# Performance work log

Hardware: AMD Instinct MI355X
Metric: run time of the kernel (lower is better)

Reference implementation:

```python
import jax, jax.numpy as jnp
import numpy as np

EPS = 1e-9
# exp factors for iterations i = 4,3,2,1,0,-1,-2 ; i == -2 -> 0.0
EXP_FACTORS = np.array([-(4.0 ** i) if i != -2 else 0.0 for i in range(4, -3, -1)], dtype=np.float32)


def setup_inputs() -> dict:
    key = jax.random.key(0)
    k1, k2 = jax.random.split(key)
    B, N, D = 16, 2048, 256
    preds = jax.random.normal(k1, (B, N, D), dtype=jnp.float32)
    labels = jax.random.normal(k2, (B, N, D), dtype=jnp.float32)
    return {"preds": preds, "labels": labels}


def _pairwise_dist(p1, p2):
    # [B,N,1] + [B,1,N] - 2 * p1 @ p2^T -> [B,N,N]
    p1_norm = jnp.sum(p1 * p1, axis=-1)[..., :, None]
    p2_norm = jnp.sum(p2 * p2, axis=-1)[..., None, :]
    return p1_norm + p2_norm - 2.0 * jnp.einsum('bnd,bmd->bnm', p1, p2)


def _approx_match(pwdist):
    B, N, _ = pwdist.shape
    match0 = jnp.zeros_like(pwdist)
    currency0 = jnp.ones((B, N, 1), dtype=pwdist.dtype)
    cost0 = jnp.ones((B, 1, N), dtype=pwdist.dtype)

    def body(carry, exp_factor):
        match, cost, currency = carry
        bids = jnp.exp(exp_factor * pwdist) * cost              # [B,N,N]
        bids = bids * currency / (jnp.sum(bids, axis=2, keepdims=True) + EPS)
        bid_wt = jnp.minimum(cost / (jnp.sum(bids, axis=1, keepdims=True) + EPS), 1.0)
        bids = bids * bid_wt
        match = match + bids
        cost = jnp.maximum(cost - jnp.sum(bids, axis=1, keepdims=True), 0.0)
        currency = jnp.maximum(currency - jnp.sum(bids, axis=2, keepdims=True), 0.0)
        return (match, cost, currency), None

    (match, _, _), _ = jax.lax.scan(body, (match0, cost0, currency0), jnp.asarray(EXP_FACTORS))
    return match


def reference(preds, labels):
    pwdist = _pairwise_dist(preds, labels)
    match = _approx_match(pwdist)
    return jnp.sum(match * pwdist)
```

## Files before the change

### kernel.cpp

```cpp
#include <hip/hip_runtime.h>
#include <cstdint>

#define B_ 16
#define N_ 2048
#define D_ 256
#define EPS_ 1e-9f

#define AS1 __attribute__((address_space(1)))
#define AS3 __attribute__((address_space(3)))

typedef float f4 __attribute__((ext_vector_type(4)));
typedef __attribute__((ext_vector_type(8))) short short8;

__device__ inline unsigned short f2bf(float x){
  unsigned int u = __float_as_uint(x);
  u = (u + 0x7fffu + ((u >> 16) & 1u)) >> 16;
  return (unsigned short)u;
}
__device__ inline float bf2f(unsigned short u){
  return __uint_as_float(((unsigned int)u) << 16);
}

__device__ float blockReduceSum(float x, float* red){
  int tid = threadIdx.x;
  red[tid] = x; __syncthreads();
  #pragma unroll
  for (int off = 128; off > 0; off >>= 1){
    if (tid < off) red[tid] += red[tid + off];
    __syncthreads();
  }
  float r = red[0]; __syncthreads();
  return r;
}

__global__ __launch_bounds__(256) void prep_kernel(
    const float* __restrict__ preds, const float* __restrict__ labels,
    unsigned short* __restrict__ pabf, unsigned short* __restrict__ pbbf,
    float* __restrict__ pn, float* __restrict__ ln,
    float* __restrict__ cost, float* __restrict__ currency,
    int* __restrict__ dmin, float* __restrict__ PL,
    float* __restrict__ scal, float* __restrict__ out){
  int s = blockIdx.y;
  if (s == 0){
    int i = blockIdx.x * 256 + threadIdx.x;
    if (i < B_ * N_){ cost[i] = 1.f; currency[i] = 1.f; }
    if (i < 2 * B_ * D_) PL[i] = 0.f;
    if (i < B_ * 4) scal[i] = 0.f;
    if (i < B_) dmin[i] = 0x7f7fffff;
    if (i == 0) out[0] = 0.f;
  }
  const float* src = s ? labels : preds;
  unsigned short* dst = s ? pbbf : pabf;
  float* norms = s ? ln : pn;
  int gw = (blockIdx.x * blockDim.x + threadIdx.x) >> 6;
  int lane = threadIdx.x & 63;
  const float4 v = ((const float4*)(src + (size_t)gw * D_))[lane];
  float sum = v.x*v.x + v.y*v.y + v.z*v.z + v.w*v.w;
  #pragma unroll
  for (int off = 32; off >= 1; off >>= 1) sum += __shfl_xor(sum, off);
  if (lane == 0) norms[gw] = sum;
  ushort4 o; o.x = f2bf(v.x); o.y = f2bf(v.y); o.z = f2bf(v.z); o.w = f2bf(v.w);
  ((ushort4*)(dst + (size_t)gw * D_))[lane] = o;
}

__global__ __launch_bounds__(512, 2) void gemm_minmax(
    const unsigned short* __restrict__ pa, const unsigned short* __restrict__ pbm,
    const float* __restrict__ pn, const float* __restrict__ ln,
    int* __restrict__ dmin)
{
  int lid = blockIdx.x;
  int l = lid >> 3;
  int b = 2 * (lid & 7) + (l >> 6);
  int t = l & 63;
  int tm = (t & 7) * 256, tn = (t >> 3) * 256;
  const unsigned short* A  = pa  + (size_t)b * N_ * D_;
  const unsigned short* Bm = pbm + (size_t)b * N_ * D_;
  __shared__ __align__(16) unsigned short As[2][256 * 64];
  __shared__ __align__(16) unsigned short Bs[2][256 * 64];
  __shared__ float minred[8];
  int tid = threadIdx.x, lane = tid & 63, w = tid >> 6;
  int wm = (w >> 2) * 128, wn = (w & 3) * 64;
  int quad = lane >> 4, l15 = lane & 15;

  f4 acc[8][4];
  #pragma unroll
  for (int i = 0; i < 8; i++)
    #pragma unroll
    for (int j = 0; j < 4; j++) acc[i][j] = (f4)0.f;

  int lr = lane >> 3, ch = lane & 7;
  int gch = (ch ^ lr) * 8;

  #pragma unroll
  for (int p = 0; p < 4; p++){
    int R = p * 64 + w * 8;
    int r = R + lr;
    __builtin_amdgcn_global_load_lds(
        (const AS1 unsigned int*)(const void*)&A[(size_t)(tm + r) * D_ + gch],
        (AS3 unsigned int*)(void*)&As[0][R * 64], 16, 0, 0);
    __builtin_amdgcn_global_load_lds(
        (const AS1 unsigned int*)(const void*)&Bm[(size_t)(tn + r) * D_ + gch],
        (AS3 unsigned int*)(void*)&Bs[0][R * 64], 16, 0, 0);
  }

  int buf = 0;
  for (int ki = 0; ki < 4; ki++){
    __syncthreads();
    if (ki < 3){
      int kt = (ki + 1) * 64;
      #pragma unroll
      for (int p = 0; p < 4; p++){
        int R = p * 64 + w * 8;
        int r = R + lr;
        __builtin_amdgcn_global_load_lds(
            (const AS1 unsigned int*)(const void*)&A[(size_t)(tm + r) * D_ + kt + gch],
            (AS3 unsigned int*)(void*)&As[buf ^ 1][R * 64], 16, 0, 0);
        __builtin_amdgcn_global_load_lds(
            (const AS1 unsigned int*)(const void*)&Bm[(size_t)(tn + r) * D_ + kt + gch],
            (AS3 unsigned int*)(void*)&Bs[buf ^ 1][R * 64], 16, 0, 0);
      }
    }
    #pragma unroll
    for (int ks = 0; ks < 2; ks++){
      short8 af[8], bf[4];
      int j = ks * 4 + quad;
      #pragma unroll
      for (int i = 0; i < 8; i++){
        int ra = wm + i * 16 + l15;
        af[i] = *(const short8*)(&As[buf][ra * 64 + ((j ^ (ra & 7)) * 8)]);
      }
      #pragma unroll
      for (int jj = 0; jj < 4; jj++){
        int rb = wn + jj * 16 + l15;
        bf[jj] = *(const short8*)(&Bs[buf][rb * 64 + ((j ^ (rb & 7)) * 8)]);
      }
      #pragma unroll
      for (int i = 0; i < 8; i++)
        #pragma unroll
        for (int jj = 0; jj < 4; jj++)
          acc[i][jj] = __builtin_amdgcn_mfma_f32_16x16x32_bf16(af[i], bf[jj], acc[i][jj], 0, 0, 0);
    }
    buf ^= 1;
  }

  float4 pnr[8];
  float lnr[4];
  #pragma unroll
  for (int i = 0; i < 8; i++)
    pnr[i] = *(const float4*)&pn[(size_t)b * N_ + tm + wm + i * 16 + quad * 4];
  #pragma unroll
  for (int jj = 0; jj < 4; jj++)
    lnr[jj] = ln[(size_t)b * N_ + tn + wn + jj * 16 + l15];

  float mind = 3.4e38f;
  #pragma unroll
  for (int i = 0; i < 8; i++){
    float pv[4] = {pnr[i].x, pnr[i].y, pnr[i].z, pnr[i].w};
    #pragma unroll
    for (int jj = 0; jj < 4; jj++){
      #pragma unroll
      for (int reg = 0; reg < 4; reg++){
        float v = pv[reg] + lnr[jj] - 2.f * acc[i][jj][reg];
        mind = fminf(mind, v);
      }
    }
  }
  #pragma unroll
  for (int off = 32; off >= 1; off >>= 1) mind = fminf(mind, __shfl_xor(mind, off));
  if (lane == 0) minred[w] = mind;
  __syncthreads();
  if (tid == 0){
    float m = minred[0];
    #pragma unroll
    for (int q = 1; q < 8; q++) m = fminf(m, minred[q]);
    atomicMin(&dmin[b], __float_as_int(fmaxf(m, 0.f)));
  }
}

__global__ __launch_bounds__(256) void fb_all(
    const unsigned short* __restrict__ pabf, const unsigned short* __restrict__ pbbf,
    const float* __restrict__ pn, const float* __restrict__ ln,
    float* __restrict__ cost, float* __restrict__ currency,
    const int* __restrict__ dmin, float* __restrict__ out,
    float* __restrict__ alpha, float* __restrict__ v, float* __restrict__ scal)
{
  const float EF[6] = {-256.f, -64.f, -16.f, -4.f, -1.f, -0.25f};
  int b = blockIdx.x, tid = threadIdx.x;
  float dm = __int_as_float(dmin[b]);
  __shared__ float red[256];
  __shared__ float alpha_l[N_];
  __shared__ float prow[D_];
  const unsigned short* A  = pabf + (size_t)b * N_ * D_;
  const unsigned short* Bm = pbbf + (size_t)b * N_ * D_;
  const float* pnb = pn + (size_t)b * N_;
  const float* lnb = ln + (size_t)b * N_;
  float* costb = cost + (size_t)b * N_;
  float* curb  = currency + (size_t)b * N_;
  for (int it = 0; it < 6; it++){
    float ef = EF[it];
    if (ef * (dm - 8.f) < -55.f) continue;
    float cost_c[8], colsum_c[8], bw_c[8], costnew_c[8];
    #pragma unroll
    for (int j = 0; j < 8; j++){ cost_c[j] = costb[j*256+tid]; colsum_c[j] = 0.f; }
    for (int r = 0; r < N_; r++){
      prow[tid] = bf2f(A[(size_t)r * D_ + tid]);
      __syncthreads();
      float s_c[8], rs = 0.f;
      for (int j = 0; j < 8; j++){
        int m = j*256+tid; float dot = 0.f;
        for (int k = 0; k < D_; k++) dot += prow[k] * bf2f(Bm[(size_t)m * D_ + k]);
        float d = pnb[r] + lnb[m] - 2.f*dot;
        float s = __expf(ef * d) * cost_c[j];
        s_c[j] = s; rs += s;
      }
      float tot = blockReduceSum(rs, red);
      float a = curb[r] / (tot + EPS_);
      if (tid == 0) alpha_l[r] = a;
      #pragma unroll
      for (int j = 0; j < 8; j++) colsum_c[j] += s_c[j] * a;
      __syncthreads();
    }
    #pragma unroll
    for (int j = 0; j < 8; j++){
      float cs = colsum_c[j];
      float bw = fminf(cost_c[j] / (cs + EPS_), 1.f);
      bw_c[j] = bw; costnew_c[j] = fmaxf(cost_c[j] - bw*cs, 0.f);
    }
    float contrib = 0.f;
    for (int r = 0; r < N_; r++){
      prow[tid] = bf2f(A[(size_t)r * D_ + tid]);
      __syncthreads();
      float a = alpha_l[r], rbs = 0.f;
      for (int j = 0; j < 8; j++){
        int m = j*256+tid; float dot = 0.f;
        for (int k = 0; k < D_; k++) dot += prow[k] * bf2f(Bm[(size_t)m * D_ + k]);
        float d = pnb[r] + lnb[m] - 2.f*dot;
        float bid = __expf(ef * d) * cost_c[j] * a * bw_c[j];
        rbs += bid; contrib += bid * d;
      }
      float tot = blockReduceSum(rbs, red);
      if (tid == 0) curb[r] = fmaxf(curb[r] - tot, 0.f);
      __syncthreads();
    }
    #pragma unroll
    for (int j = 0; j < 8; j++) costb[j*256+tid] = costnew_c[j];
    float ctot = blockReduceSum(contrib, red);
    if (tid == 0) atomicAdd(out, ctot);
    __syncthreads();
  }
  float* ab = alpha + (size_t)b * N_;
  float* vb = v + (size_t)b * N_;
  float s = 0.f;
  #pragma unroll
  for (int j = 0; j < 8; j++) s += costb[j*256+tid];
  float Sc = blockReduceSum(s, red);
  float sa = 0.f, spn = 0.f;
  #pragma unroll
  for (int j = 0; j < 8; j++){
    int i = j*256+tid;
    float a = curb[i] / (Sc + EPS_);
    ab[i] = a; sa += a; spn += a * pnb[i];
  }
  float Sa  = blockReduceSum(sa, red);
  float Spn = blockReduceSum(spn, red);
  float sv = 0.f, sln = 0.f;
  #pragma unroll
  for (int j = 0; j < 8; j++){
    int i = j*256+tid;
    float c = costb[j*256+tid];
    float bw = fminf(c / (c * Sa + EPS_), 1.f);
    float vv = c * bw;
    vb[i] = vv; sv += vv; sln += vv * lnb[i];
  }
  float Sv  = blockReduceSum(sv, red);
  float Sln = blockReduceSum(sln, red);
  if (tid == 0){
    scal[b*4+0] = Sa; scal[b*4+1] = Sv; scal[b*4+2] = Spn; scal[b*4+3] = Sln;
  }
}

__global__ __launch_bounds__(256) void cf_wsum(
    const unsigned short* __restrict__ pabf, const unsigned short* __restrict__ pbbf,
    const float* __restrict__ alpha, const float* __restrict__ v,
    float* __restrict__ PL)
{
  int chunk = blockIdx.x, src = blockIdx.y, b = blockIdx.z, tid = threadIdx.x;
  int g = tid >> 6, c4 = (tid & 63) * 4;
  const unsigned short* X = (src ? pbbf : pabf) + ((size_t)b * N_ + chunk * 64) * D_;
  const float* wv = (src ? v : alpha) + (size_t)b * N_ + chunk * 64;
  __shared__ float wl[64];
  __shared__ float part[4][D_];
  if (tid < 64) wl[tid] = wv[tid];
  __syncthreads();
  f4 acc = (f4)0.f;
  for (int r = g * 16; r < g * 16 + 16; r++){
    uint2 pk = *(const uint2*)&X[(size_t)r * D_ + c4];
    float wr = wl[r];
    acc[0] = fmaf(wr, __uint_as_float(pk.x << 16), acc[0]);
    acc[1] = fmaf(wr, __uint_as_float(pk.x & 0xffff0000u), acc[1]);
    acc[2] = fmaf(wr, __uint_as_float(pk.y << 16), acc[2]);
    acc[3] = fmaf(wr, __uint_as_float(pk.y & 0xffff0000u), acc[3]);
  }
  #pragma unroll
  for (int q = 0; q < 4; q++) part[g][c4 + q] = acc[q];
  __syncthreads();
  float s = part[0][tid] + part[1][tid] + part[2][tid] + part[3][tid];
  atomicAdd(&PL[((size_t)src * B_ + b) * D_ + tid], s);
}

__global__ __launch_bounds__(256) void cf_final(
    const float* __restrict__ PL, const float* __restrict__ scal,
    float* __restrict__ out)
{
  int b = blockIdx.x, tid = threadIdx.x;
  __shared__ float red[256];
  float p = PL[(size_t)b * D_ + tid] * PL[((size_t)B_ + b) * D_ + tid];
  float dot = blockReduceSum(p, red);
  if (tid == 0){
    float Sa = scal[b*4+0], Sv = scal[b*4+1], Spn = scal[b*4+2], Sln = scal[b*4+3];
    atomicAdd(out, Spn * Sv + Sa * Sln - 2.f * dot);
  }
}

extern "C" void kernel_launch(void* const* d_in, const int* in_sizes, int n_in,
                              void* d_out, int out_size, void* d_ws, size_t ws_size,
                              hipStream_t stream)
{
  const float* preds  = (const float*)d_in[0];
  const float* labels = (const float*)d_in[1];
  float* out = (float*)d_out;
  char* ws = (char*)d_ws;
  const size_t BN = (size_t)B_ * N_;
  size_t off = 0;
  float* cost     = (float*)(ws + off); off += BN * 4;
  float* currency = (float*)(ws + off); off += BN * 4;
  float* alpha    = (float*)(ws + off); off += BN * 4;
  float* v        = (float*)(ws + off); off += BN * 4;
  float* pn       = (float*)(ws + off); off += BN * 4;
  float* ln       = (float*)(ws + off); off += BN * 4;
  int*   dmin     = (int*)(ws + off);   off += 256;
  float* scal     = (float*)(ws + off); off += 256;
  float* PL       = (float*)(ws + off); off += (size_t)2 * B_ * D_ * 4;
  unsigned short* pabf = (unsigned short*)(ws + off); off += BN * D_ * 2;
  unsigned short* pbbf = (unsigned short*)(ws + off); off += BN * D_ * 2;

  prep_kernel<<<dim3((unsigned)(BN / 4), 2), 256, 0, stream>>>(
      preds, labels, pabf, pbbf, pn, ln, cost, currency, dmin, PL, scal, out);
  gemm_minmax<<<dim3(1024), 512, 0, stream>>>(pabf, pbbf, pn, ln, dmin);
  fb_all<<<dim3(B_), 256, 0, stream>>>(pabf, pbbf, pn, ln, cost, currency, dmin, out,
                                       alpha, v, scal);
  cf_wsum<<<dim3(32, 2, B_), 256, 0, stream>>>(pabf, pbbf, alpha, v, PL);
  cf_final<<<dim3(B_), 256, 0, stream>>>(PL, scal, out);
}
```

Baseline: 150.3 us.

## Persist GEMM blocks across four column tiles and batch rows in prep kernel

```diff
diff --git a/kernel.cpp b/kernel.cpp
--- a/kernel.cpp
+++ b/kernel.cpp
@@ -41,8 +41,9 @@
     int* __restrict__ dmin, float* __restrict__ PL,
     float* __restrict__ scal, float* __restrict__ out){
   int s = blockIdx.y;
+  int tid = threadIdx.x;
   if (s == 0){
-    int i = blockIdx.x * 256 + threadIdx.x;
+    int i = blockIdx.x * 256 + tid;
     if (i < B_ * N_){ cost[i] = 1.f; currency[i] = 1.f; }
     if (i < 2 * B_ * D_) PL[i] = 0.f;
     if (i < B_ * 4) scal[i] = 0.f;
@@ -52,27 +53,35 @@
   const float* src = s ? labels : preds;
   unsigned short* dst = s ? pbbf : pabf;
   float* norms = s ? ln : pn;
-  int gw = (blockIdx.x * blockDim.x + threadIdx.x) >> 6;
-  int lane = threadIdx.x & 63;
-  const float4 v = ((const float4*)(src + (size_t)gw * D_))[lane];
-  float sum = v.x*v.x + v.y*v.y + v.z*v.z + v.w*v.w;
-  #pragma unroll
-  for (int off = 32; off >= 1; off >>= 1) sum += __shfl_xor(sum, off);
-  if (lane == 0) norms[gw] = sum;
-  ushort4 o; o.x = f2bf(v.x); o.y = f2bf(v.y); o.z = f2bf(v.z); o.w = f2bf(v.w);
-  ((ushort4*)(dst + (size_t)gw * D_))[lane] = o;
-}
-
-__global__ __launch_bounds__(512, 2) void gemm_minmax(
+  int wid = (blockIdx.x * 256 + tid) >> 6;
+  int lane = tid & 63;
+  size_t row0 = (size_t)wid * 4;
+  float4 v[4];
+  #pragma unroll
+  for (int q = 0; q < 4; q++)
+    v[q] = ((const float4*)(src + (row0 + q) * D_))[lane];
+  #pragma unroll
+  for (int q = 0; q < 4; q++){
+    float sum = v[q].x*v[q].x + v[q].y*v[q].y + v[q].z*v[q].z + v[q].w*v[q].w;
+    #pragma unroll
+    for (int off = 32; off >= 1; off >>= 1) sum += __shfl_xor(sum, off);
+    if (lane == 0) norms[row0 + q] = sum;
+    ushort4 o; o.x = f2bf(v[q].x); o.y = f2bf(v[q].y); o.z = f2bf(v[q].z); o.w = f2bf(v[q].w);
+    ((ushort4*)(dst + (row0 + q) * D_))[lane] = o;
+  }
+}
+
+__global__ __launch_bounds__(512) void gemm_minmax(
     const unsigned short* __restrict__ pa, const unsigned short* __restrict__ pbm,
     const float* __restrict__ pn, const float* __restrict__ ln,
     int* __restrict__ dmin)
 {
   int lid = blockIdx.x;
-  int l = lid >> 3;
-  int b = 2 * (lid & 7) + (l >> 6);
-  int t = l & 63;
-  int tm = (t & 7) * 256, tn = (t >> 3) * 256;
+  int xcd = lid & 7, sq = lid >> 3;
+  int b = 2 * xcd + (sq >> 4);
+  int rest = sq & 15;
+  int tm = (rest >> 1) * 256;
+  int tnh = rest & 1;
   const unsigned short* A  = pa  + (size_t)b * N_ * D_;
   const unsigned short* Bm = pbm + (size_t)b * N_ * D_;
   __shared__ __align__(16) unsigned short As[2][256 * 64];
@@ -91,35 +100,38 @@
   int lr = lane >> 3, ch = lane & 7;
   int gch = (ch ^ lr) * 8;
 
-  #pragma unroll
-  for (int p = 0; p < 4; p++){
-    int R = p * 64 + w * 8;
-    int r = R + lr;
-    __builtin_amdgcn_global_load_lds(
-        (const AS1 unsigned int*)(const void*)&A[(size_t)(tm + r) * D_ + gch],
-        (AS3 unsigned int*)(void*)&As[0][R * 64], 16, 0, 0);
-    __builtin_amdgcn_global_load_lds(
-        (const AS1 unsigned int*)(const void*)&Bm[(size_t)(tn + r) * D_ + gch],
-        (AS3 unsigned int*)(void*)&Bs[0][R * 64], 16, 0, 0);
-  }
-
-  int buf = 0;
-  for (int ki = 0; ki < 4; ki++){
+  auto load_stage = [&](int st){
+    int ti = st >> 2, ki = st & 3;
+    int tn = (tnh * 4 + ti) * 256;
+    int kt = ki * 64;
+    int bufI = st & 1;
+    #pragma unroll
+    for (int p = 0; p < 4; p++){
+      int R = p * 64 + w * 8;
+      int r = R + lr;
+      __builtin_amdgcn_global_load_lds(
+          (const AS1 unsigned int*)(const void*)&A[(size_t)(tm + r) * D_ + kt + gch],
+          (AS3 unsigned int*)(void*)&As[bufI][R * 64], 16, 0, 0);
+      __builtin_amdgcn_global_load_lds(
+          (const AS1 unsigned int*)(const void*)&Bm[(size_t)(tn + r) * D_ + kt + gch],
+          (AS3 unsigned int*)(void*)&Bs[bufI][R * 64], 16, 0, 0);
+    }
+  };
+
+  load_stage(0);
+  float lnr[4];
+  float mind = 3.4e38f;
+  for (int st = 0; st < 16; st++){
     __syncthreads();
-    if (ki < 3){
-      int kt = (ki + 1) * 64;
-      #pragma unroll
-      for (int p = 0; p < 4; p++){
-        int R = p * 64 + w * 8;
-        int r = R + lr;
-        __builtin_amdgcn_global_load_lds(
-            (const AS1 unsigned int*)(const void*)&A[(size_t)(tm + r) * D_ + kt + gch],
-            (AS3 unsigned int*)(void*)&As[buf ^ 1][R * 64], 16, 0, 0);
-        __builtin_amdgcn_global_load_lds(
-            (const AS1 unsigned int*)(const void*)&Bm[(size_t)(tn + r) * D_ + kt + gch],
-            (AS3 unsigned int*)(void*)&Bs[buf ^ 1][R * 64], 16, 0, 0);
-      }
-    }
+    if (st < 15) load_stage(st + 1);
+    int ki = st & 3;
+    if (ki == 0){
+      int tn = (tnh * 4 + (st >> 2)) * 256;
+      #pragma unroll
+      for (int jj = 0; jj < 4; jj++)
+        lnr[jj] = ln[(size_t)b * N_ + tn + wn + jj * 16 + l15];
+    }
+    int buf = st & 1;
     #pragma unroll
     for (int ks = 0; ks < 2; ks++){
       short8 af[8], bf[4];
@@ -140,31 +152,24 @@
         for (int jj = 0; jj < 4; jj++)
           acc[i][jj] = __builtin_amdgcn_mfma_f32_16x16x32_bf16(af[i], bf[jj], acc[i][jj], 0, 0, 0);
     }
-    buf ^= 1;
-  }
-
-  float4 pnr[8];
-  float lnr[4];
-  #pragma unroll
-  for (int i = 0; i < 8; i++)
-    pnr[i] = *(const float4*)&pn[(size_t)b * N_ + tm + wm + i * 16 + quad * 4];
-  #pragma unroll
-  for (int jj = 0; jj < 4; jj++)
-    lnr[jj] = ln[(size_t)b * N_ + tn + wn + jj * 16 + l15];
-
-  float mind = 3.4e38f;
-  #pragma unroll
-  for (int i = 0; i < 8; i++){
-    float pv[4] = {pnr[i].x, pnr[i].y, pnr[i].z, pnr[i].w};
-    #pragma unroll
-    for (int jj = 0; jj < 4; jj++){
-      #pragma unroll
-      for (int reg = 0; reg < 4; reg++){
-        float v = pv[reg] + lnr[jj] - 2.f * acc[i][jj][reg];
-        mind = fminf(mind, v);
-      }
-    }
-  }
+    if (ki == 3){
+      #pragma unroll
+      for (int i = 0; i < 8; i++){
+        float4 pv4 = *(const float4*)&pn[(size_t)b * N_ + tm + wm + i * 16 + quad * 4];
+        float pv[4] = {pv4.x, pv4.y, pv4.z, pv4.w};
+        #pragma unroll
+        for (int jj = 0; jj < 4; jj++){
+          #pragma unroll
+          for (int reg = 0; reg < 4; reg++){
+            float v = pv[reg] + lnr[jj] - 2.f * acc[i][jj][reg];
+            mind = fminf(mind, v);
+            acc[i][jj][reg] = 0.f;
+          }
+        }
+      }
+    }
+  }
+
   #pragma unroll
   for (int off = 32; off >= 1; off >>= 1) mind = fminf(mind, __shfl_xor(mind, off));
   if (lane == 0) minred[w] = mind;
@@ -344,9 +349,9 @@
   unsigned short* pabf = (unsigned short*)(ws + off); off += BN * D_ * 2;
   unsigned short* pbbf = (unsigned short*)(ws + off); off += BN * D_ * 2;
 
-  prep_kernel<<<dim3((unsigned)(BN / 4), 2), 256, 0, stream>>>(
+  prep_kernel<<<dim3((unsigned)(BN / 16), 2), 256, 0, stream>>>(
       preds, labels, pabf, pbbf, pn, ln, cost, currency, dmin, PL, scal, out);
-  gemm_minmax<<<dim3(1024), 512, 0, stream>>>(pabf, pbbf, pn, ln, dmin);
+  gemm_minmax<<<dim3(256), 512, 0, stream>>>(pabf, pbbf, pn, ln, dmin);
   fb_all<<<dim3(B_), 256, 0, stream>>>(pabf, pbbf, pn, ln, cost, currency, dmin, out,
                                        alpha, v, scal);
   cf_wsum<<<dim3(32, 2, B_), 256, 0, stream>>>(pabf, pbbf, alpha, v, PL);
```

After: 152.4 us. About the same (+1.4%).

## Fuse final weighted-sum reduction into prep column sums with fast uniform path

Applied to the files above, without the earlier changes.

```diff
diff --git a/kernel.cpp b/kernel.cpp
--- a/kernel.cpp
+++ b/kernel.cpp
@@ -38,29 +38,55 @@
     unsigned short* __restrict__ pabf, unsigned short* __restrict__ pbbf,
     float* __restrict__ pn, float* __restrict__ ln,
     float* __restrict__ cost, float* __restrict__ currency,
-    int* __restrict__ dmin, float* __restrict__ PL,
-    float* __restrict__ scal, float* __restrict__ out){
+    int* __restrict__ dmin, float* __restrict__ Ppart,
+    float* __restrict__ npart){
   int s = blockIdx.y;
+  int tid = threadIdx.x;
   if (s == 0){
-    int i = blockIdx.x * 256 + threadIdx.x;
+    int i = blockIdx.x * 256 + tid;
     if (i < B_ * N_){ cost[i] = 1.f; currency[i] = 1.f; }
-    if (i < 2 * B_ * D_) PL[i] = 0.f;
-    if (i < B_ * 4) scal[i] = 0.f;
     if (i < B_) dmin[i] = 0x7f7fffff;
-    if (i == 0) out[0] = 0.f;
   }
   const float* src = s ? labels : preds;
   unsigned short* dst = s ? pbbf : pabf;
   float* norms = s ? ln : pn;
-  int gw = (blockIdx.x * blockDim.x + threadIdx.x) >> 6;
-  int lane = threadIdx.x & 63;
-  const float4 v = ((const float4*)(src + (size_t)gw * D_))[lane];
-  float sum = v.x*v.x + v.y*v.y + v.z*v.z + v.w*v.w;
-  #pragma unroll
-  for (int off = 32; off >= 1; off >>= 1) sum += __shfl_xor(sum, off);
-  if (lane == 0) norms[gw] = sum;
-  ushort4 o; o.x = f2bf(v.x); o.y = f2bf(v.y); o.z = f2bf(v.z); o.w = f2bf(v.w);
-  ((ushort4*)(dst + (size_t)gw * D_))[lane] = o;
+  int w = tid >> 6, lane = tid & 63;
+  size_t row0 = (size_t)blockIdx.x * 16 + (size_t)w * 4;
+  float4 v[4];
+  #pragma unroll
+  for (int q = 0; q < 4; q++)
+    v[q] = ((const float4*)(src + (row0 + q) * D_))[lane];
+  __shared__ f4 part[4][64];
+  __shared__ float nred[4];
+  f4 s4;
+  s4[0] = v[0].x + v[1].x + v[2].x + v[3].x;
+  s4[1] = v[0].y + v[1].y + v[2].y + v[3].y;
+  s4[2] = v[0].z + v[1].z + v[2].z + v[3].z;
+  s4[3] = v[0].w + v[1].w + v[2].w + v[3].w;
+  float nsum = 0.f;
+  #pragma unroll
+  for (int q = 0; q < 4; q++){
+    float sum = v[q].x*v[q].x + v[q].y*v[q].y + v[q].z*v[q].z + v[q].w*v[q].w;
+    #pragma unroll
+    for (int off = 32; off >= 1; off >>= 1) sum += __shfl_xor(sum, off);
+    if (lane == 0){ norms[row0 + q] = sum; nsum += sum; }
+    ushort4 o; o.x = f2bf(v[q].x); o.y = f2bf(v[q].y); o.z = f2bf(v[q].z); o.w = f2bf(v[q].w);
+    ((ushort4*)(dst + (row0 + q) * D_))[lane] = o;
+  }
+  part[w][lane] = s4;
+  if (lane == 0) nred[w] = nsum;
+  __syncthreads();
+  if (tid < 64){
+    f4 t = part[0][tid];
+    #pragma unroll
+    for (int q = 1; q < 4; q++){
+      t[0] += part[q][tid][0]; t[1] += part[q][tid][1];
+      t[2] += part[q][tid][2]; t[3] += part[q][tid][3];
+    }
+    *(f4*)(Ppart + ((size_t)s * 2048 + blockIdx.x) * 256 + tid * 4) = t;
+  }
+  if (tid == 0)
+    npart[s * 2048 + blockIdx.x] = nred[0] + nred[1] + nred[2] + nred[3];
 }
 
 __global__ __launch_bounds__(512, 2) void gemm_minmax(
@@ -181,8 +207,7 @@
     const unsigned short* __restrict__ pabf, const unsigned short* __restrict__ pbbf,
     const float* __restrict__ pn, const float* __restrict__ ln,
     float* __restrict__ cost, float* __restrict__ currency,
-    const int* __restrict__ dmin, float* __restrict__ out,
-    float* __restrict__ alpha, float* __restrict__ v, float* __restrict__ scal)
+    const int* __restrict__ dmin, float* __restrict__ out)
 {
   const float EF[6] = {-256.f, -64.f, -16.f, -4.f, -1.f, -0.25f};
   int b = blockIdx.x, tid = threadIdx.x;
@@ -248,8 +273,39 @@
     if (tid == 0) atomicAdd(out, ctot);
     __syncthreads();
   }
-  float* ab = alpha + (size_t)b * N_;
-  float* vb = v + (size_t)b * N_;
+}
+
+__global__ __launch_bounds__(256) void finalize(
+    const unsigned short* __restrict__ pabf, const unsigned short* __restrict__ pbbf,
+    const float* __restrict__ pn, const float* __restrict__ ln,
+    const float* __restrict__ cost, const float* __restrict__ currency,
+    const int* __restrict__ dmin, const float* __restrict__ Ppart,
+    const float* __restrict__ npart, float* __restrict__ out)
+{
+  int b = blockIdx.x, tid = threadIdx.x;
+  __shared__ float red[256];
+  float dm = __int_as_float(dmin[b]);
+  if (-0.25f * (dm - 8.f) < -55.f){
+    float Pc = 0.f, Lc = 0.f;
+    for (int k = 0; k < 128; k++){
+      Pc += Ppart[((size_t)b * 128 + k) * 256 + tid];
+      Lc += Ppart[((size_t)(2048 + b * 128 + k)) * 256 + tid];
+    }
+    float np = (tid < 128) ? npart[b * 128 + tid] : 0.f;
+    float nl = (tid < 128) ? npart[2048 + b * 128 + tid] : 0.f;
+    float Spn = blockReduceSum(np, red);
+    float Sln = blockReduceSum(nl, red);
+    float dot = blockReduceSum(Pc * Lc, red);
+    if (tid == 0) atomicAdd(out, Spn + Sln - dot * (1.f / 1024.f));
+    return;
+  }
+  __shared__ float warr[N_];
+  const unsigned short* A  = pabf + (size_t)b * N_ * D_;
+  const unsigned short* Bm = pbbf + (size_t)b * N_ * D_;
+  const float* pnb = pn + (size_t)b * N_;
+  const float* lnb = ln + (size_t)b * N_;
+  const float* costb = cost + (size_t)b * N_;
+  const float* curb  = currency + (size_t)b * N_;
   float s = 0.f;
   #pragma unroll
   for (int j = 0; j < 8; j++) s += costb[j*256+tid];
@@ -259,67 +315,30 @@
   for (int j = 0; j < 8; j++){
     int i = j*256+tid;
     float a = curb[i] / (Sc + EPS_);
-    ab[i] = a; sa += a; spn += a * pnb[i];
+    warr[i] = a; sa += a; spn += a * pnb[i];
   }
   float Sa  = blockReduceSum(sa, red);
   float Spn = blockReduceSum(spn, red);
+  float Pc = 0.f;
+  for (int r = 0; r < N_; r++)
+    Pc += warr[r] * bf2f(A[(size_t)r * D_ + tid]);
+  __syncthreads();
   float sv = 0.f, sln = 0.f;
   #pragma unroll
   for (int j = 0; j < 8; j++){
     int i = j*256+tid;
-    float c = costb[j*256+tid];
+    float c = costb[i];
     float bw = fminf(c / (c * Sa + EPS_), 1.f);
     float vv = c * bw;
-    vb[i] = vv; sv += vv; sln += vv * lnb[i];
+    warr[i] = vv; sv += vv; sln += vv * lnb[i];
   }
   float Sv  = blockReduceSum(sv, red);
   float Sln = blockReduceSum(sln, red);
-  if (tid == 0){
-    scal[b*4+0] = Sa; scal[b*4+1] = Sv; scal[b*4+2] = Spn; scal[b*4+3] = Sln;
-  }
-}
-
-__global__ __launch_bounds__(256) void cf_wsum(
-    const unsigned short* __restrict__ pabf, const unsigned short* __restrict__ pbbf,
-    const float* __restrict__ alpha, const float* __restrict__ v,
-    float* __restrict__ PL)
-{
-  int chunk = blockIdx.x, src = blockIdx.y, b = blockIdx.z, tid = threadIdx.x;
-  int g = tid >> 6, c4 = (tid & 63) * 4;
-  const unsigned short* X = (src ? pbbf : pabf) + ((size_t)b * N_ + chunk * 64) * D_;
-  const float* wv = (src ? v : alpha) + (size_t)b * N_ + chunk * 64;
-  __shared__ float wl[64];
-  __shared__ float part[4][D_];
-  if (tid < 64) wl[tid] = wv[tid];
-  __syncthreads();
-  f4 acc = (f4)0.f;
-  for (int r = g * 16; r < g * 16 + 16; r++){
-    uint2 pk = *(const uint2*)&X[(size_t)r * D_ + c4];
-    float wr = wl[r];
-    acc[0] = fmaf(wr, __uint_as_float(pk.x << 16), acc[0]);
-    acc[1] = fmaf(wr, __uint_as_float(pk.x & 0xffff0000u), acc[1]);
-    acc[2] = fmaf(wr, __uint_as_float(pk.y << 16), acc[2]);
-    acc[3] = fmaf(wr, __uint_as_float(pk.y & 0xffff0000u), acc[3]);
-  }
-  #pragma unroll
-  for (int q = 0; q < 4; q++) part[g][c4 + q] = acc[q];
-  __syncthreads();
-  float s = part[0][tid] + part[1][tid] + part[2][tid] + part[3][tid];
-  atomicAdd(&PL[((size_t)src * B_ + b) * D_ + tid], s);
-}
-
-__global__ __launch_bounds__(256) void cf_final(
-    const float* __restrict__ PL, const float* __restrict__ scal,
-    float* __restrict__ out)
-{
-  int b = blockIdx.x, tid = threadIdx.x;
-  __shared__ float red[256];
-  float p = PL[(size_t)b * D_ + tid] * PL[((size_t)B_ + b) * D_ + tid];
-  float dot = blockReduceSum(p, red);
-  if (tid == 0){
-    float Sa = scal[b*4+0], Sv = scal[b*4+1], Spn = scal[b*4+2], Sln = scal[b*4+3];
-    atomicAdd(out, Spn * Sv + Sa * Sln - 2.f * dot);
-  }
+  float Lc = 0.f;
+  for (int m = 0; m < N_; m++)
+    Lc += warr[m] * bf2f(Bm[(size_t)m * D_ + tid]);
+  float dot = blockReduceSum(Pc * Lc, red);
+  if (tid == 0) atomicAdd(out, Spn * Sv + Sa * Sln - 2.f * dot);
 }
 
 extern "C" void kernel_launch(void* const* d_in, const int* in_sizes, int n_in,
@@ -334,21 +353,19 @@
   size_t off = 0;
   float* cost     = (float*)(ws + off); off += BN * 4;
   float* currency = (float*)(ws + off); off += BN * 4;
-  float* alpha    = (float*)(ws + off); off += BN * 4;
-  float* v        = (float*)(ws + off); off += BN * 4;
   float* pn       = (float*)(ws + off); off += BN * 4;
   float* ln       = (float*)(ws + off); off += BN * 4;
   int*   dmin     = (int*)(ws + off);   off += 256;
-  float* scal     = (float*)(ws + off); off += 256;
-  float* PL       = (float*)(ws + off); off += (size_t)2 * B_ * D_ * 4;
+  float* npart    = (float*)(ws + off); off += (size_t)2 * 2048 * 4;
+  float* Ppart    = (float*)(ws + off); off += (size_t)2 * 2048 * 256 * 4;
   unsigned short* pabf = (unsigned short*)(ws + off); off += BN * D_ * 2;
   unsigned short* pbbf = (unsigned short*)(ws + off); off += BN * D_ * 2;
 
-  prep_kernel<<<dim3((unsigned)(BN / 4), 2), 256, 0, stream>>>(
-      preds, labels, pabf, pbbf, pn, ln, cost, currency, dmin, PL, scal, out);
+  hipMemsetAsync(d_out, 0, 4, stream);
+  prep_kernel<<<dim3((unsigned)(BN / 16), 2), 256, 0, stream>>>(
+      preds, labels, pabf, pbbf, pn, ln, cost, currency, dmin, Ppart, npart);
   gemm_minmax<<<dim3(1024), 512, 0, stream>>>(pabf, pbbf, pn, ln, dmin);
-  fb_all<<<dim3(B_), 256, 0, stream>>>(pabf, pbbf, pn, ln, cost, currency, dmin, out,
-                                       alpha, v, scal);
-  cf_wsum<<<dim3(32, 2, B_), 256, 0, stream>>>(pabf, pbbf, alpha, v, PL);
-  cf_final<<<dim3(B_), 256, 0, stream>>>(PL, scal, out);
-}
+  fb_all<<<dim3(B_), 256, 0, stream>>>(pabf, pbbf, pn, ln, cost, currency, dmin, out);
+  finalize<<<dim3(B_), 256, 0, stream>>>(pabf, pbbf, pn, ln, cost, currency, dmin,
+                                         Ppart, npart, out);
+}
```

Result: no change. 148.8 us (-1.0%).
